# Optimization experiments

Measured on AMD Instinct MI355X. Metric: run time of the kernel, lower is better.

The kernel has to match this reference:

```python
import jax, jax.numpy as jnp
import numpy as np

H = 1024


def _gru_dir(xg, h0, w_hh, b_hh, reverse):
    # xg: (L, G, 3H) precomputed input-gate projections; h0: (G, H)
    def step(h, xt):
        hg = h @ w_hh.T + b_hh
        xr, xz, xn = jnp.split(xt, 3, axis=-1)
        hr, hz, hn = jnp.split(hg, 3, axis=-1)
        r = jax.nn.sigmoid(xr + hr)
        z = jax.nn.sigmoid(xz + hz)
        n = jnp.tanh(xn + r * hn)
        h_new = (1.0 - z) * n + z * h
        return h_new, h_new
    _, hs = jax.lax.scan(step, h0, xg, reverse=reverse)
    return hs  # (L, G, H), time-ordered (scan reverse keeps original order)


def setup_inputs() -> dict:
    key = jax.random.key(0)
    ks = jax.random.split(key, 12)
    N, G, L = 16384, 256, 128
    s = 1.0 / np.sqrt(H)
    inp = {
        "h_atom": jax.random.normal(ks[0], (N, H), dtype=jnp.float32),
        "batch": jnp.sort(jax.random.randint(ks[1], (N,), 0, G)),
        "bias": jax.random.uniform(ks[2], (H,), jnp.float32, -s, s),
        "w_ih_f": jax.random.uniform(ks[3], (3 * H, H), jnp.float32, -s, s),
        "w_hh_f": jax.random.uniform(ks[4], (3 * H, H), jnp.float32, -s, s),
        "b_ih_f": jax.random.uniform(ks[5], (3 * H,), jnp.float32, -s, s),
        "b_hh_f": jax.random.uniform(ks[6], (3 * H,), jnp.float32, -s, s),
        "w_ih_b": jax.random.uniform(ks[7], (3 * H, H), jnp.float32, -s, s),
        "w_hh_b": jax.random.uniform(ks[8], (3 * H, H), jnp.float32, -s, s),
        "b_ih_b": jax.random.uniform(ks[9], (3 * H,), jnp.float32, -s, s),
        "b_hh_b": jax.random.uniform(ks[10], (3 * H,), jnp.float32, -s, s),
        "num_graphs": G,
        "pad_len": L,
    }
    return inp


def reference(h_atom, bias, w_ih_f, w_hh_f, b_ih_f, b_hh_f,
              w_ih_b, w_hh_b, b_ih_b, b_hh_b, batch, num_graphs, pad_len):
    N = h_atom.shape[0]
    G, L = num_graphs, pad_len
    message = jax.nn.relu(h_atom + bias)  # (N, H)

    # per-graph counts / positions (batch is sorted by graph id)
    counts = jax.ops.segment_sum(jnp.ones((N,), jnp.int32), batch, num_segments=G)
    start = jnp.cumsum(counts) - counts
    pos = jnp.arange(N) - start[batch]  # position of each atom within its graph

    # pad ragged atoms -> (G, L, H); padded slots stay zero (matches torch)
    msgs = jnp.zeros((G, L, H), h_atom.dtype).at[batch, pos].set(message)

    # segment-max hidden init, shared by both directions
    h0 = jax.ops.segment_max(h_atom, batch, num_segments=G)  # (G, H)
    h0 = jnp.where(counts[:, None] > 0, h0, 0.0)

    # precompute input-gate projections, time-major
    xg_f = jnp.einsum('glh,kh->lgk', msgs, w_ih_f) + b_ih_f  # (L, G, 3H)
    xg_b = jnp.einsum('glh,kh->lgk', msgs, w_ih_b) + b_ih_b

    hs_f = _gru_dir(xg_f, h0, w_hh_f, b_hh_f, reverse=False)  # (L, G, H)
    hs_b = _gru_dir(xg_b, h0, w_hh_b, b_hh_b, reverse=True)   # (L, G, H)

    h_messages = jnp.concatenate([hs_f, hs_b], axis=-1).transpose(1, 0, 2)  # (G, L, 2H)

    # unpad back to (N, 2H)
    return h_messages[batch, pos]
```

## Files before the change

kernel.cpp:

```cpp
#include <hip/hip_runtime.h>
#include <stdint.h>

#define H 1024
#define G_ 256
#define LPAD 128

typedef float  floatx4 __attribute__((ext_vector_type(4)));
typedef short  shortx8 __attribute__((ext_vector_type(8)));

#define MFMA(a, b, c) __builtin_amdgcn_mfma_f32_16x16x32_bf16((a), (b), (c), 0, 0, 0)

__device__ __forceinline__ uint16_t f2bf(float f) {
  union { float f; uint32_t i; } v; v.f = f;
  uint32_t r = (v.i + 0x7FFFu + ((v.i >> 16) & 1u)) >> 16;
  return (uint16_t)r;
}
__device__ __forceinline__ float bf2f(uint16_t u) {
  union { uint32_t i; float f; } v; v.i = ((uint32_t)u) << 16; return v.f;
}
__device__ __forceinline__ float sigmoid_(float x) { return 1.f / (1.f + __expf(-x)); }
__device__ __forceinline__ float tanh_(float x) {
  float ax = fabsf(x);
  float e = __expf(2.f * ax);
  float t = 1.f - 2.f / (e + 1.f);
  return x >= 0.f ? t : -t;
}

__global__ void k_f2b(const float* __restrict__ src, uint16_t* __restrict__ dst) {
  size_t i = ((size_t)blockIdx.x * blockDim.x + threadIdx.x) * 8;
  float4 a = *(const float4*)(src + i);
  float4 b = *(const float4*)(src + i + 4);
  uint16_t o[8] = {f2bf(a.x), f2bf(a.y), f2bf(a.z), f2bf(a.w),
                   f2bf(b.x), f2bf(b.y), f2bf(b.z), f2bf(b.w)};
  uint4 ov; __builtin_memcpy(&ov, o, 16);
  *(uint4*)(dst + i) = ov;
}

__global__ void k_setup(const int* __restrict__ batch, int N, int* __restrict__ start) {
  int g = threadIdx.x;
  if (g > G_) return;
  int lo = 0, hi = N;
  while (lo < hi) { int mid = (lo + hi) >> 1; if (batch[mid] < g) lo = mid + 1; else hi = mid; }
  start[g] = lo;
}

__global__ void k_msg(const float* __restrict__ h_atom, const float* __restrict__ bias,
                      uint16_t* __restrict__ msg) {
  int row = blockIdx.x, t = threadIdx.x;
  size_t off = (size_t)row * H + t * 8;
  float4 h0 = *(const float4*)(h_atom + off);
  float4 h1 = *(const float4*)(h_atom + off + 4);
  float4 b0 = *(const float4*)(bias + t * 8);
  float4 b1 = *(const float4*)(bias + t * 8 + 4);
  float v[8] = {h0.x + b0.x, h0.y + b0.y, h0.z + b0.z, h0.w + b0.w,
                h1.x + b1.x, h1.y + b1.y, h1.z + b1.z, h1.w + b1.w};
  uint16_t o[8];
#pragma unroll
  for (int i = 0; i < 8; i++) o[i] = f2bf(v[i] > 0.f ? v[i] : 0.f);
  uint4 ov; __builtin_memcpy(&ov, o, 16);
  *(uint4*)(msg + off) = ov;
}

__global__ void k_h0(const float* __restrict__ h_atom, const int* __restrict__ start,
                     float* __restrict__ hf32, uint16_t* __restrict__ hbf) {
  int g = blockIdx.x, t = threadIdx.x;
  int s = start[g], e = start[g + 1];
  float m[4] = {-INFINITY, -INFINITY, -INFINITY, -INFINITY};
  const float* base = h_atom + t * 4;
  for (int a = s; a < e; a++) {
    float4 v = *(const float4*)(base + (size_t)a * H);
    m[0] = fmaxf(m[0], v.x); m[1] = fmaxf(m[1], v.y);
    m[2] = fmaxf(m[2], v.z); m[3] = fmaxf(m[3], v.w);
  }
  if (s == e) { m[0] = m[1] = m[2] = m[3] = 0.f; }
#pragma unroll
  for (int i = 0; i < 4; i++) {
    int c = t * 4 + i;
    float mv = m[i];
    uint16_t bv = f2bf(mv);
    hf32[(size_t)0 * G_ * H + (size_t)g * H + c] = mv;
    hf32[(size_t)2 * G_ * H + (size_t)g * H + c] = mv;
    hbf [(size_t)0 * G_ * H + (size_t)g * H + c] = bv;
    hbf [(size_t)2 * G_ * H + (size_t)g * H + c] = bv;
  }
}

__global__ __launch_bounds__(256) void k_gemm_xg(
    const uint16_t* __restrict__ A, const uint16_t* __restrict__ Wf,
    const uint16_t* __restrict__ Wb, uint16_t* __restrict__ C, int N) {
  __shared__ __align__(16) uint16_t As[128 * 64];
  __shared__ __align__(16) uint16_t Bs[128 * 64];
  int bn = blockIdx.x, bm = blockIdx.y;
  const uint16_t* B = (bn < 24) ? Wf : Wb;
  int brow = (bn < 24 ? bn : bn - 24) * 128;
  int tid = threadIdx.x, wid = tid >> 6, lane = tid & 63;
  int wm = wid >> 1, wn = wid & 1;
  floatx4 acc[4][4];
#pragma unroll
  for (int mi = 0; mi < 4; mi++)
#pragma unroll
    for (int ni = 0; ni < 4; ni++) acc[mi][ni] = (floatx4){0.f, 0.f, 0.f, 0.f};
  int arow = bm * 128;
  for (int kb = 0; kb < H; kb += 64) {
    uint4 av[4], bv[4];
#pragma unroll
    for (int p = 0; p < 4; p++) {
      int c = p * 256 + tid;
      av[p] = *(const uint4*)(A + (size_t)(arow + (c >> 3)) * H + kb + (c & 7) * 8);
      bv[p] = *(const uint4*)(B + (size_t)(brow + (c >> 3)) * H + kb + (c & 7) * 8);
    }
    __syncthreads();
#pragma unroll
    for (int p = 0; p < 4; p++) {
      int c = p * 256 + tid;
      *(uint4*)(As + (size_t)c * 8) = av[p];
      *(uint4*)(Bs + (size_t)c * 8) = bv[p];
    }
    __syncthreads();
#pragma unroll
    for (int ks = 0; ks < 2; ks++) {
      const uint16_t* ab = As + ((wm * 64 + (lane & 15)) * 64 + ks * 32 + (lane >> 4) * 8);
      const uint16_t* bb = Bs + ((wn * 64 + (lane & 15)) * 64 + ks * 32 + (lane >> 4) * 8);
      shortx8 af[4], bfr[4];
#pragma unroll
      for (int i = 0; i < 4; i++) {
        af[i]  = *(const shortx8*)(ab + i * 16 * 64);
        bfr[i] = *(const shortx8*)(bb + i * 16 * 64);
      }
#pragma unroll
      for (int mi = 0; mi < 4; mi++)
#pragma unroll
        for (int ni = 0; ni < 4; ni++)
          acc[mi][ni] = MFMA(af[mi], bfr[ni], acc[mi][ni]);
    }
  }
  int colb = bn * 128 + wn * 64 + (lane & 15);
  int rowb = bm * 128 + wm * 64 + (lane >> 4) * 4;
#pragma unroll
  for (int mi = 0; mi < 4; mi++)
#pragma unroll
    for (int ni = 0; ni < 4; ni++) {
      size_t base = (size_t)(rowb + mi * 16) * 6144 + colb + ni * 16;
#pragma unroll
      for (int r = 0; r < 4; r++) C[base + (size_t)r * 6144] = f2bf(acc[mi][ni][r]);
    }
}

__global__ __launch_bounds__(256) void k_step(
    int l, const uint16_t* __restrict__ xg,
    const uint16_t* __restrict__ whf, const uint16_t* __restrict__ whb,
    const float* __restrict__ bihf, const float* __restrict__ bhhf,
    const float* __restrict__ bihb, const float* __restrict__ bhhb,
    float* __restrict__ hf32, uint16_t* __restrict__ hbf,
    const int* __restrict__ start, float* __restrict__ out) {
  __shared__ __align__(16) uint16_t As[64 * 64];
  __shared__ __align__(16) uint16_t Bs[96 * 64];
  __shared__ float HG[64 * 97];
  int b = blockIdx.x;
  int e = b & 7, hi = b >> 3;
  int d = e >> 2, jm = e & 3;
  int jc = (hi & 7) * 4 + jm;
  int g0 = (hi >> 3) * 64;
  int cur = l & 1;
  const uint16_t* W = d ? whb : whf;
  const uint16_t* hsrc = hbf + (size_t)(d * 2 + cur) * G_ * H;
  int tid = threadIdx.x, wid = tid >> 6, lane = tid & 63;
  int wm = wid >> 1, wn = wid & 1;
  floatx4 acc[2][3];
#pragma unroll
  for (int mi = 0; mi < 2; mi++)
#pragma unroll
    for (int ni = 0; ni < 3; ni++) acc[mi][ni] = (floatx4){0.f, 0.f, 0.f, 0.f};

  for (int kb = 0; kb < H; kb += 64) {
    uint4 av[2], bv[3];
#pragma unroll
    for (int p = 0; p < 2; p++) {
      int c = p * 256 + tid;
      av[p] = *(const uint4*)(hsrc + (size_t)(g0 + (c >> 3)) * H + kb + (c & 7) * 8);
    }
#pragma unroll
    for (int p = 0; p < 3; p++) {
      int c = p * 256 + tid;
      int row = c >> 3;
      int wrow = (row >> 5) * H + jc * 32 + (row & 31);
      bv[p] = *(const uint4*)(W + (size_t)wrow * H + kb + (c & 7) * 8);
    }
    __syncthreads();
#pragma unroll
    for (int p = 0; p < 2; p++) *(uint4*)(As + (size_t)(p * 256 + tid) * 8) = av[p];
#pragma unroll
    for (int p = 0; p < 3; p++) *(uint4*)(Bs + (size_t)(p * 256 + tid) * 8) = bv[p];
    __syncthreads();
#pragma unroll
    for (int ks = 0; ks < 2; ks++) {
      const uint16_t* ab = As + ((wm * 32 + (lane & 15)) * 64 + ks * 32 + (lane >> 4) * 8);
      const uint16_t* bb = Bs + ((wn * 48 + (lane & 15)) * 64 + ks * 32 + (lane >> 4) * 8);
      shortx8 a0 = *(const shortx8*)ab;
      shortx8 a1 = *(const shortx8*)(ab + 16 * 64);
#pragma unroll
      for (int ni = 0; ni < 3; ni++) {
        shortx8 bvf = *(const shortx8*)(bb + ni * 16 * 64);
        acc[0][ni] = MFMA(a0, bvf, acc[0][ni]);
        acc[1][ni] = MFMA(a1, bvf, acc[1][ni]);
      }
    }
  }
  __syncthreads();
#pragma unroll
  for (int mi = 0; mi < 2; mi++)
#pragma unroll
    for (int ni = 0; ni < 3; ni++) {
      int row0 = wm * 32 + mi * 16 + (lane >> 4) * 4;
      int col = wn * 48 + ni * 16 + (lane & 15);
#pragma unroll
      for (int r = 0; r < 4; r++) HG[(row0 + r) * 97 + col] = acc[mi][ni][r];
    }
  __syncthreads();

  int base = tid * 8;
  int gl = base >> 5, j0 = base & 31;
  int g = g0 + gl;
  int s = start[g], cnt = start[g + 1] - s;
  int t = d ? (LPAD - 1 - l) : l;
  bool active = (t < cnt);
  int col0 = jc * 32 + j0;
  const float* bih = d ? bihb : bihf;
  const float* bhh = d ? bhhb : bhhf;
  const uint16_t* xp = xg + (size_t)(s + t) * 6144 + (size_t)d * 3072;
  const float* h_old = hf32 + ((size_t)(d * 2 + cur) * G_ + g) * H + col0;
  float* h_new32 = hf32 + ((size_t)(d * 2 + (cur ^ 1)) * G_ + g) * H + col0;
  uint16_t* h_newb = hbf + ((size_t)(d * 2 + (cur ^ 1)) * G_ + g) * H + col0;
  float* op = out + (size_t)(s + t) * 2048 + (size_t)d * H + col0;
#pragma unroll
  for (int i = 0; i < 8; i++) {
    int c = col0 + i;
    float hr = HG[gl * 97 + j0 + i];
    float hz = HG[gl * 97 + 32 + j0 + i];
    float hn = HG[gl * 97 + 64 + j0 + i];
    float xr = 0.f, xz = 0.f, xn = 0.f;
    if (active) { xr = bf2f(xp[c]); xz = bf2f(xp[H + c]); xn = bf2f(xp[2 * H + c]); }
    float r = sigmoid_(xr + bih[c] + hr + bhh[c]);
    float z = sigmoid_(xz + bih[H + c] + hz + bhh[H + c]);
    float n = tanh_(xn + bih[2 * H + c] + r * (hn + bhh[2 * H + c]));
    float hv = h_old[i];
    float hnew = (1.f - z) * n + z * hv;
    h_new32[i] = hnew;
    h_newb[i] = f2bf(hnew);
    if (active) op[i] = hnew;
  }
}

extern "C" void kernel_launch(void* const* d_in, const int* in_sizes, int n_in,
                              void* d_out, int out_size, void* d_ws, size_t ws_size,
                              hipStream_t stream) {
  const float* h_atom = (const float*)d_in[0];
  const int*   batch  = (const int*)d_in[1];
  const float* bias   = (const float*)d_in[2];
  const float* w_ih_f = (const float*)d_in[3];
  const float* w_hh_f = (const float*)d_in[4];
  const float* b_ih_f = (const float*)d_in[5];
  const float* b_hh_f = (const float*)d_in[6];
  const float* w_ih_b = (const float*)d_in[7];
  const float* w_hh_b = (const float*)d_in[8];
  const float* b_ih_b = (const float*)d_in[9];
  const float* b_hh_b = (const float*)d_in[10];
  int N = in_sizes[0] / H;
  float* out = (float*)d_out;

  const size_t W3 = (size_t)3 * H * H;
  char* ws = (char*)d_ws;
  uint16_t* msg  = (uint16_t*)ws;
  uint16_t* xg   = (uint16_t*)(ws + (size_t)N * H * 2);
  char* p = ws + (size_t)N * H * 2 + (size_t)N * 6144 * 2;
  uint16_t* wihf = (uint16_t*)p; p += W3 * 2;
  uint16_t* wihb = (uint16_t*)p; p += W3 * 2;
  uint16_t* whhf = (uint16_t*)p; p += W3 * 2;
  uint16_t* whhb = (uint16_t*)p; p += W3 * 2;
  float*    hf32 = (float*)p;    p += (size_t)4 * G_ * H * 4;
  uint16_t* hbf  = (uint16_t*)p; p += (size_t)4 * G_ * H * 2;
  int*      start = (int*)p;

  int wgrid = (int)(W3 / (256 * 8));
  k_f2b<<<wgrid, 256, 0, stream>>>(w_ih_f, wihf);
  k_f2b<<<wgrid, 256, 0, stream>>>(w_ih_b, wihb);
  k_f2b<<<wgrid, 256, 0, stream>>>(w_hh_f, whhf);
  k_f2b<<<wgrid, 256, 0, stream>>>(w_hh_b, whhb);
  k_setup<<<1, 512, 0, stream>>>(batch, N, start);
  k_msg<<<N, 128, 0, stream>>>(h_atom, bias, msg);
  k_h0<<<G_, 256, 0, stream>>>(h_atom, start, hf32, hbf);
  k_gemm_xg<<<dim3(48, N / 128), 256, 0, stream>>>(msg, wihf, wihb, xg, N);
  for (int l = 0; l < LPAD; l++)
    k_step<<<256, 256, 0, stream>>>(l, xg, whhf, whhb, b_ih_f, b_hh_f,
                                    b_ih_b, b_hh_b, hf32, hbf, start, out);
}
```

Baseline: 8.251 ms.

## Fuse recurrent GRU steps into one persistent cooperative kernel with grid barrier

Replaces the 128 per-timestep kernel launches with a single cooperative persistent kernel that loops over timesteps and synchronizes all 256 blocks through an atomic-counter grid barrier. The barrier counter is reset in the setup kernel. The aim is to remove launch overhead and inter-kernel gaps on the serial recurrence. It also stages the input-projection GEMM epilogue through shared memory so output stores are coalesced 16-byte writes. The cost is spin-waiting on a global atomic each step, and correctness depends on all blocks being co-resident.

```diff
diff --git a/kernel.cpp b/kernel.cpp
--- a/kernel.cpp
+++ b/kernel.cpp
@@ -36,8 +36,10 @@
   *(uint4*)(dst + i) = ov;
 }
 
-__global__ void k_setup(const int* __restrict__ batch, int N, int* __restrict__ start) {
+__global__ void k_setup(const int* __restrict__ batch, int N, int* __restrict__ start,
+                        int* __restrict__ bar) {
   int g = threadIdx.x;
+  if (g == 0) *bar = 0;
   if (g > G_) return;
   int lo = 0, hi = N;
   while (lo < hi) { int mid = (lo + hi) >> 1; if (batch[mid] < g) lo = mid + 1; else hi = mid; }
@@ -88,8 +90,9 @@
 __global__ __launch_bounds__(256) void k_gemm_xg(
     const uint16_t* __restrict__ A, const uint16_t* __restrict__ Wf,
     const uint16_t* __restrict__ Wb, uint16_t* __restrict__ C, int N) {
-  __shared__ __align__(16) uint16_t As[128 * 64];
-  __shared__ __align__(16) uint16_t Bs[128 * 64];
+  __shared__ __align__(16) uint16_t SM[128 * 128];
+  uint16_t* As = SM;
+  uint16_t* Bs = SM + 128 * 64;
   int bn = blockIdx.x, bm = blockIdx.y;
   const uint16_t* B = (bn < 24) ? Wf : Wb;
   int brow = (bn < 24 ? bn : bn - 24) * 128;
@@ -134,120 +137,144 @@
           acc[mi][ni] = MFMA(af[mi], bfr[ni], acc[mi][ni]);
     }
   }
-  int colb = bn * 128 + wn * 64 + (lane & 15);
-  int rowb = bm * 128 + wm * 64 + (lane >> 4) * 4;
+  __syncthreads();
+  int crow = wm * 64 + (lane >> 4) * 4;
+  int ccol = wn * 64 + (lane & 15);
 #pragma unroll
   for (int mi = 0; mi < 4; mi++)
 #pragma unroll
-    for (int ni = 0; ni < 4; ni++) {
-      size_t base = (size_t)(rowb + mi * 16) * 6144 + colb + ni * 16;
-#pragma unroll
-      for (int r = 0; r < 4; r++) C[base + (size_t)r * 6144] = f2bf(acc[mi][ni][r]);
-    }
-}
-
-__global__ __launch_bounds__(256) void k_step(
-    int l, const uint16_t* __restrict__ xg,
+    for (int ni = 0; ni < 4; ni++)
+#pragma unroll
+      for (int r = 0; r < 4; r++)
+        SM[(crow + mi * 16 + r) * 128 + ccol + ni * 16] = f2bf(acc[mi][ni][r]);
+  __syncthreads();
+#pragma unroll
+  for (int p = 0; p < 8; p++) {
+    int c = p * 256 + tid;
+    int row = c >> 4, col = (c & 15) * 8;
+    *(uint4*)(C + (size_t)(arow + row) * 6144 + bn * 128 + col) =
+        *(const uint4*)(SM + row * 128 + col);
+  }
+}
+
+__global__ __launch_bounds__(256) void k_gru(
+    const uint16_t* __restrict__ xg,
     const uint16_t* __restrict__ whf, const uint16_t* __restrict__ whb,
     const float* __restrict__ bihf, const float* __restrict__ bhhf,
     const float* __restrict__ bihb, const float* __restrict__ bhhb,
     float* __restrict__ hf32, uint16_t* __restrict__ hbf,
-    const int* __restrict__ start, float* __restrict__ out) {
+    const int* __restrict__ start, float* __restrict__ out,
+    int* bar) {
   __shared__ __align__(16) uint16_t As[64 * 64];
   __shared__ __align__(16) uint16_t Bs[96 * 64];
   __shared__ float HG[64 * 97];
   int b = blockIdx.x;
-  int e = b & 7, hi = b >> 3;
+  int e = b & 7, hib = b >> 3;
   int d = e >> 2, jm = e & 3;
-  int jc = (hi & 7) * 4 + jm;
-  int g0 = (hi >> 3) * 64;
-  int cur = l & 1;
+  int jc = (hib & 7) * 4 + jm;
+  int g0 = (hib >> 3) * 64;
   const uint16_t* W = d ? whb : whf;
-  const uint16_t* hsrc = hbf + (size_t)(d * 2 + cur) * G_ * H;
   int tid = threadIdx.x, wid = tid >> 6, lane = tid & 63;
   int wm = wid >> 1, wn = wid & 1;
-  floatx4 acc[2][3];
-#pragma unroll
-  for (int mi = 0; mi < 2; mi++)
-#pragma unroll
-    for (int ni = 0; ni < 3; ni++) acc[mi][ni] = (floatx4){0.f, 0.f, 0.f, 0.f};
-
-  for (int kb = 0; kb < H; kb += 64) {
-    uint4 av[2], bv[3];
-#pragma unroll
-    for (int p = 0; p < 2; p++) {
-      int c = p * 256 + tid;
-      av[p] = *(const uint4*)(hsrc + (size_t)(g0 + (c >> 3)) * H + kb + (c & 7) * 8);
-    }
-#pragma unroll
-    for (int p = 0; p < 3; p++) {
-      int c = p * 256 + tid;
-      int row = c >> 3;
-      int wrow = (row >> 5) * H + jc * 32 + (row & 31);
-      bv[p] = *(const uint4*)(W + (size_t)wrow * H + kb + (c & 7) * 8);
-    }
-    __syncthreads();
-#pragma unroll
-    for (int p = 0; p < 2; p++) *(uint4*)(As + (size_t)(p * 256 + tid) * 8) = av[p];
-#pragma unroll
-    for (int p = 0; p < 3; p++) *(uint4*)(Bs + (size_t)(p * 256 + tid) * 8) = bv[p];
-    __syncthreads();
-#pragma unroll
-    for (int ks = 0; ks < 2; ks++) {
-      const uint16_t* ab = As + ((wm * 32 + (lane & 15)) * 64 + ks * 32 + (lane >> 4) * 8);
-      const uint16_t* bb = Bs + ((wn * 48 + (lane & 15)) * 64 + ks * 32 + (lane >> 4) * 8);
-      shortx8 a0 = *(const shortx8*)ab;
-      shortx8 a1 = *(const shortx8*)(ab + 16 * 64);
-#pragma unroll
-      for (int ni = 0; ni < 3; ni++) {
-        shortx8 bvf = *(const shortx8*)(bb + ni * 16 * 64);
-        acc[0][ni] = MFMA(a0, bvf, acc[0][ni]);
-        acc[1][ni] = MFMA(a1, bvf, acc[1][ni]);
-      }
-    }
-  }
-  __syncthreads();
-#pragma unroll
-  for (int mi = 0; mi < 2; mi++)
-#pragma unroll
-    for (int ni = 0; ni < 3; ni++) {
-      int row0 = wm * 32 + mi * 16 + (lane >> 4) * 4;
-      int col = wn * 48 + ni * 16 + (lane & 15);
-#pragma unroll
-      for (int r = 0; r < 4; r++) HG[(row0 + r) * 97 + col] = acc[mi][ni][r];
-    }
-  __syncthreads();
 
   int base = tid * 8;
   int gl = base >> 5, j0 = base & 31;
   int g = g0 + gl;
   int s = start[g], cnt = start[g + 1] - s;
-  int t = d ? (LPAD - 1 - l) : l;
-  bool active = (t < cnt);
   int col0 = jc * 32 + j0;
   const float* bih = d ? bihb : bihf;
   const float* bhh = d ? bhhb : bhhf;
-  const uint16_t* xp = xg + (size_t)(s + t) * 6144 + (size_t)d * 3072;
-  const float* h_old = hf32 + ((size_t)(d * 2 + cur) * G_ + g) * H + col0;
-  float* h_new32 = hf32 + ((size_t)(d * 2 + (cur ^ 1)) * G_ + g) * H + col0;
-  uint16_t* h_newb = hbf + ((size_t)(d * 2 + (cur ^ 1)) * G_ + g) * H + col0;
-  float* op = out + (size_t)(s + t) * 2048 + (size_t)d * H + col0;
-#pragma unroll
-  for (int i = 0; i < 8; i++) {
-    int c = col0 + i;
-    float hr = HG[gl * 97 + j0 + i];
-    float hz = HG[gl * 97 + 32 + j0 + i];
-    float hn = HG[gl * 97 + 64 + j0 + i];
-    float xr = 0.f, xz = 0.f, xn = 0.f;
-    if (active) { xr = bf2f(xp[c]); xz = bf2f(xp[H + c]); xn = bf2f(xp[2 * H + c]); }
-    float r = sigmoid_(xr + bih[c] + hr + bhh[c]);
-    float z = sigmoid_(xz + bih[H + c] + hz + bhh[H + c]);
-    float n = tanh_(xn + bih[2 * H + c] + r * (hn + bhh[2 * H + c]));
-    float hv = h_old[i];
-    float hnew = (1.f - z) * n + z * hv;
-    h_new32[i] = hnew;
-    h_newb[i] = f2bf(hnew);
-    if (active) op[i] = hnew;
+
+  for (int l = 0; l < LPAD; l++) {
+    int cur = l & 1;
+    const uint16_t* hsrc = hbf + (size_t)(d * 2 + cur) * G_ * H;
+    floatx4 acc[2][3];
+#pragma unroll
+    for (int mi = 0; mi < 2; mi++)
+#pragma unroll
+      for (int ni = 0; ni < 3; ni++) acc[mi][ni] = (floatx4){0.f, 0.f, 0.f, 0.f};
+
+    for (int kb = 0; kb < H; kb += 64) {
+      uint4 av[2], bv[3];
+#pragma unroll
+      for (int p = 0; p < 2; p++) {
+        int c = p * 256 + tid;
+        av[p] = *(const uint4*)(hsrc + (size_t)(g0 + (c >> 3)) * H + kb + (c & 7) * 8);
+      }
+#pragma unroll
+      for (int p = 0; p < 3; p++) {
+        int c = p * 256 + tid;
+        int row = c >> 3;
+        int wrow = (row >> 5) * H + jc * 32 + (row & 31);
+        bv[p] = *(const uint4*)(W + (size_t)wrow * H + kb + (c & 7) * 8);
+      }
+      __syncthreads();
+#pragma unroll
+      for (int p = 0; p < 2; p++) *(uint4*)(As + (size_t)(p * 256 + tid) * 8) = av[p];
+#pragma unroll
+      for (int p = 0; p < 3; p++) *(uint4*)(Bs + (size_t)(p * 256 + tid) * 8) = bv[p];
+      __syncthreads();
+#pragma unroll
+      for (int ks = 0; ks < 2; ks++) {
+        const uint16_t* ab = As + ((wm * 32 + (lane & 15)) * 64 + ks * 32 + (lane >> 4) * 8);
+        const uint16_t* bb = Bs + ((wn * 48 + (lane & 15)) * 64 + ks * 32 + (lane >> 4) * 8);
+        shortx8 a0 = *(const shortx8*)ab;
+        shortx8 a1 = *(const shortx8*)(ab + 16 * 64);
+#pragma unroll
+        for (int ni = 0; ni < 3; ni++) {
+          shortx8 bvf = *(const shortx8*)(bb + ni * 16 * 64);
+          acc[0][ni] = MFMA(a0, bvf, acc[0][ni]);
+          acc[1][ni] = MFMA(a1, bvf, acc[1][ni]);
+        }
+      }
+    }
+    __syncthreads();
+#pragma unroll
+    for (int mi = 0; mi < 2; mi++)
+#pragma unroll
+      for (int ni = 0; ni < 3; ni++) {
+        int row0 = wm * 32 + mi * 16 + (lane >> 4) * 4;
+        int col = wn * 48 + ni * 16 + (lane & 15);
+#pragma unroll
+        for (int r = 0; r < 4; r++) HG[(row0 + r) * 97 + col] = acc[mi][ni][r];
+      }
+    __syncthreads();
+
+    int t = d ? (LPAD - 1 - l) : l;
+    bool active = (t < cnt);
+    const uint16_t* xp = xg + (size_t)(s + t) * 6144 + (size_t)d * 3072;
+    const float* h_old = hf32 + ((size_t)(d * 2 + cur) * G_ + g) * H + col0;
+    float* h_new32 = hf32 + ((size_t)(d * 2 + (cur ^ 1)) * G_ + g) * H + col0;
+    uint16_t* h_newb = hbf + ((size_t)(d * 2 + (cur ^ 1)) * G_ + g) * H + col0;
+    float* op = out + (size_t)(s + t) * 2048 + (size_t)d * H + col0;
+#pragma unroll
+    for (int i = 0; i < 8; i++) {
+      int c = col0 + i;
+      float hr = HG[gl * 97 + j0 + i];
+      float hz = HG[gl * 97 + 32 + j0 + i];
+      float hn = HG[gl * 97 + 64 + j0 + i];
+      float xr = 0.f, xz = 0.f, xn = 0.f;
+      if (active) { xr = bf2f(xp[c]); xz = bf2f(xp[H + c]); xn = bf2f(xp[2 * H + c]); }
+      float r = sigmoid_(xr + bih[c] + hr + bhh[c]);
+      float z = sigmoid_(xz + bih[H + c] + hz + bhh[H + c]);
+      float n = tanh_(xn + bih[2 * H + c] + r * (hn + bhh[2 * H + c]));
+      float hv = h_old[i];
+      float hnew = (1.f - z) * n + z * hv;
+      h_new32[i] = hnew;
+      h_newb[i] = f2bf(hnew);
+      if (active) op[i] = hnew;
+    }
+
+    __syncthreads();
+    if (tid == 0) {
+      __threadfence();
+      __hip_atomic_fetch_add(bar, 1, __ATOMIC_RELEASE, __HIP_MEMORY_SCOPE_AGENT);
+      int tgt = (l + 1) << 8;
+      while (__hip_atomic_load(bar, __ATOMIC_RELAXED, __HIP_MEMORY_SCOPE_AGENT) < tgt)
+        __builtin_amdgcn_s_sleep(2);
+      __threadfence();
+    }
+    __syncthreads();
   }
 }
 
@@ -280,17 +307,20 @@
   float*    hf32 = (float*)p;    p += (size_t)4 * G_ * H * 4;
   uint16_t* hbf  = (uint16_t*)p; p += (size_t)4 * G_ * H * 2;
   int*      start = (int*)p;
+  int*      bar   = (int*)(p + 2048);
 
   int wgrid = (int)(W3 / (256 * 8));
   k_f2b<<<wgrid, 256, 0, stream>>>(w_ih_f, wihf);
   k_f2b<<<wgrid, 256, 0, stream>>>(w_ih_b, wihb);
   k_f2b<<<wgrid, 256, 0, stream>>>(w_hh_f, whhf);
   k_f2b<<<wgrid, 256, 0, stream>>>(w_hh_b, whhb);
-  k_setup<<<1, 512, 0, stream>>>(batch, N, start);
+  k_setup<<<1, 512, 0, stream>>>(batch, N, start, bar);
   k_msg<<<N, 128, 0, stream>>>(h_atom, bias, msg);
   k_h0<<<G_, 256, 0, stream>>>(h_atom, start, hf32, hbf);
   k_gemm_xg<<<dim3(48, N / 128), 256, 0, stream>>>(msg, wihf, wihb, xg, N);
-  for (int l = 0; l < LPAD; l++)
-    k_step<<<256, 256, 0, stream>>>(l, xg, whhf, whhb, b_ih_f, b_hh_f,
-                                    b_ih_b, b_hh_b, hf32, hbf, start, out);
-}
+
+  void* ka[] = {(void*)&xg, (void*)&whhf, (void*)&whhb,
+                (void*)&b_ih_f, (void*)&b_hh_f, (void*)&b_ih_b, (void*)&b_hh_b,
+                (void*)&hf32, (void*)&hbf, (void*)&start, (void*)&out, (void*)&bar};
+  hipLaunchCooperativeKernel(k_gru, dim3(G_), dim3(256), ka, 0, stream);
+}
```

After: 8.876 ms. 1.08x slower.
